# Optimization experiments

Measured on AMD Instinct MI355X. Metric: run time of the kernel, lower is better.

## Reference

```python
import jax, jax.numpy as jnp
import numpy as np

HEADS = 16

def setup_inputs() -> dict:
    key = jax.random.key(0)
    k1, k2, k3, k4 = jax.random.split(key, 4)
    B, S, D = 4, 2048, 1024
    x = jax.random.normal(k1, (B, S, D), dtype=jnp.float32)
    # original inits weights to constant 0.02; use small random init scaled similarly
    # to keep softmax non-degenerate while matching the module's math exactly.
    wq = jax.random.normal(k2, (D, D), dtype=jnp.float32) * 0.02
    wk = jax.random.normal(k3, (D, D), dtype=jnp.float32) * 0.02
    wv = jax.random.normal(k4, (D, D), dtype=jnp.float32) * 0.02
    return {"x": x, "wq": wq, "wk": wk, "wv": wv}

def reference(x, wq, wk, wv):
    B, S, D = x.shape
    H = HEADS
    hd = D // H
    # project and split heads: [B, S, D] -> [B, H, S, hd]
    q = (x @ wq).reshape(B, S, H, hd).transpose(0, 2, 1, 3)
    k = (x @ wk).reshape(B, S, H, hd).transpose(0, 2, 1, 3)
    v = (x @ wv).reshape(B, S, H, hd).transpose(0, 2, 1, 3)
    scores = jnp.einsum('bhid,bhjd->bhij', q, k) / jnp.sqrt(jnp.float32(hd))
    attn = jax.nn.softmax(scores, axis=-1)
    out = jnp.einsum('bhij,bhjd->bhid', attn, v)
    return out.transpose(0, 2, 1, 3).reshape(B, S, D)
```

## Files before the change

### kernel.cpp

```cpp
#include <hip/hip_runtime.h>
#include <hip/hip_bf16.h>
#include <stdint.h>


typedef __hip_bfloat16 bf16;
typedef __attribute__((ext_vector_type(8))) short short8;
typedef __attribute__((ext_vector_type(4))) float f32x4;
typedef __attribute__((ext_vector_type(4))) unsigned int u32x4;
typedef __attribute__((ext_vector_type(8))) unsigned short ushort8;

#define MFMA_16x16x32(a, b, c) __builtin_amdgcn_mfma_f32_16x16x32_bf16((a), (b), (c), 0, 0, 0)

__device__ __forceinline__ void gload_lds16(const void* g, void* l) {
  __builtin_amdgcn_global_load_lds((const __attribute__((address_space(1))) unsigned int*)g,
                                   (__attribute__((address_space(3))) unsigned int*)l,
                                   16, 0, 0);
}

__device__ __forceinline__ unsigned short bfu(float f) {
  return __bfloat16_as_ushort(__float2bfloat16(f));
}
__device__ __forceinline__ unsigned int pack2(float lo, float hi) {
  unsigned int r;
  asm("v_cvt_pk_bf16_f32 %0, %1, %2" : "=v"(r) : "v"(lo), "v"(hi));
  return r;
}
__device__ __forceinline__ float exp2_fast(float x) {
  float r;
  asm("v_exp_f32 %0, %1" : "=v"(r) : "v"(x));
  return r;
}

__global__ __launch_bounds__(256) void cvt_all_kernel(const float* __restrict__ x,
                                                      const float* __restrict__ w0,
                                                      const float* __restrict__ w1,
                                                      const float* __restrict__ w2,
                                                      bf16* __restrict__ xbf,
                                                      bf16* __restrict__ wT) {
  __shared__ float tile[64][65];
  const int t = threadIdx.x;
  const int bid = blockIdx.x;
  if (bid < 4096) {
    int i = bid * 256 + t;
    const float4* xv = (const float4*)x;
    float4 a = xv[i * 2];
    float4 b = xv[i * 2 + 1];
    ushort8 o;
    o[0] = bfu(a.x); o[1] = bfu(a.y); o[2] = bfu(a.z); o[3] = bfu(a.w);
    o[4] = bfu(b.x); o[5] = bfu(b.y); o[6] = bfu(b.z); o[7] = bfu(b.w);
    ((ushort8*)xbf)[i] = o;
    return;
  }
  const int wb = bid - 4096;
  const int mat = wb >> 8;
  const int rem = wb & 255;
  const int k0 = (rem >> 4) * 64;
  const int n0 = (rem & 15) * 64;
  const float* w = (mat == 0) ? w0 : ((mat == 1) ? w1 : w2);
#pragma unroll
  for (int it = 0; it < 4; ++it) {
    int lin = it * 1024 + t * 4;
    int row = lin >> 6, col = lin & 63;
    float4 v = *(const float4*)&w[(size_t)(k0 + row) * 1024 + n0 + col];
    tile[row][col] = v.x; tile[row][col + 1] = v.y;
    tile[row][col + 2] = v.z; tile[row][col + 3] = v.w;
  }
  __syncthreads();
#pragma unroll
  for (int it = 0; it < 2; ++it) {
    int chunk = it * 256 + t;
    int nrow = chunk >> 3, kc = chunk & 7;
    ushort8 o;
#pragma unroll
    for (int j = 0; j < 8; ++j) o[j] = bfu(tile[kc * 8 + j][nrow]);
    *(ushort8*)&wT[((size_t)mat * 1024 + n0 + nrow) * 1024 + k0 + kc * 8] = o;
  }
}

__global__ __launch_bounds__(256) void qkv_gemm_kernel(const bf16* __restrict__ A,
                                                       const bf16* __restrict__ Wt,
                                                       bf16* __restrict__ qb,
                                                       bf16* __restrict__ kb,
                                                       bf16* __restrict__ vtb) {
  __shared__ bf16 As[128 * 32];
  __shared__ bf16 Bs[128 * 32];
  const int t = threadIdx.x;
  const int w = t >> 6;
  const int lane = t & 63;
  const int G = lane >> 4, lq = lane & 15;
  const int m0 = blockIdx.y * 128;
  const int n0 = blockIdx.x * 128;
  const int wr = w >> 1, wc = w & 1;

  const f32x4 fzero = {0.f, 0.f, 0.f, 0.f};
  f32x4 acc[4][4];
#pragma unroll
  for (int i = 0; i < 4; ++i)
#pragma unroll
    for (int j = 0; j < 4; ++j) acc[i][j] = fzero;

  const int crow = t >> 2;
  const int ckc = t & 3;

  for (int k0 = 0; k0 < 1024; k0 += 32) {
#pragma unroll
    for (int rep = 0; rep < 2; ++rep) {
      int row = rep * 64 + crow;
      gload_lds16(&A[(size_t)(m0 + row) * 1024 + k0 + ckc * 8],
                  &As[(size_t)(rep * 256 + w * 64) * 8]);
      gload_lds16(&Wt[(size_t)(n0 + row) * 1024 + k0 + ckc * 8],
                  &Bs[(size_t)(rep * 256 + w * 64) * 8]);
    }
    __syncthreads();
    short8 af[4], bfr[4];
#pragma unroll
    for (int i = 0; i < 4; ++i)
      af[i] = *(const short8*)&As[(wr * 64 + i * 16 + lq) * 32 + G * 8];
#pragma unroll
    for (int j = 0; j < 4; ++j)
      bfr[j] = *(const short8*)&Bs[(wc * 64 + j * 16 + lq) * 32 + G * 8];
#pragma unroll
    for (int i = 0; i < 4; ++i)
#pragma unroll
      for (int j = 0; j < 4; ++j)
        acc[i][j] = MFMA_16x16x32(af[i], bfr[j], acc[i][j]);
    __syncthreads();
  }

  const int matid = n0 >> 10;
  const int nb = n0 & 1023;
#pragma unroll
  for (int i = 0; i < 4; ++i) {
#pragma unroll
    for (int r = 0; r < 4; ++r) {
      int mm = m0 + wr * 64 + i * 16 + G * 4 + r;
      int b = mm >> 11, s = mm & 2047;
#pragma unroll
      for (int j = 0; j < 4; ++j) {
        int nn = nb + wc * 64 + j * 16 + lq;
        int h = nn >> 6, d = nn & 63;
        float c = acc[i][j][r];
        size_t pb = (size_t)(b * 16 + h);
        if (matid == 0)
          qb[(pb * 2048 + s) * 64 + d] = __float2bfloat16(c * 0.18033688011112f);
        else if (matid == 1)
          kb[(pb * 2048 + s) * 64 + d] = __float2bfloat16(c);
        else
          vtb[(pb * 64 + d) * 2048 + s] = __float2bfloat16(c);
      }
    }
  }
}

__global__ __launch_bounds__(256) void attn_kernel(const bf16* __restrict__ Q,
                                                   const bf16* __restrict__ K,
                                                   const bf16* __restrict__ VT,
                                                   float* __restrict__ O) {
  __shared__ bf16 Kb[2][4096];
  __shared__ bf16 Vb[2][4096];
  const int t = threadIdx.x;
  const int w = t >> 6, lane = t & 63;
  const int G = lane >> 4, lq = lane & 15;
  const int sw = lq & 7;
  const int bid = blockIdx.x;
  const int pair = (((bid >> 7) & 7) << 3) | (bid & 7);
  const int chunk = (bid >> 3) & 15;
  const int b = pair >> 4, h = pair & 15;
  const size_t base = (size_t)pair * (2048 * 64);
  const int q0 = chunk * 128 + w * 32;

  const f32x4 fzero = {0.f, 0.f, 0.f, 0.f};
  short8 ones;
#pragma unroll
  for (int j = 0; j < 8; ++j) ones[j] = (short)0x3F80;

  const int srow = t >> 3, sbc = t & 7;
  const int ssc = (sbc ^ (srow & 7)) * 8;
  const int kprow = ((srow & 12) << 1) | ((srow & 16) >> 2) | (srow & 3);

#define STAGE_TILE(kvbase, bufi)                                                   \
  do {                                                                             \
    gload_lds16(&K[base + (size_t)((kvbase) + kprow) * 64 + ssc],                  \
                &Kb[bufi][(size_t)(w * 64) * 8]);                                  \
    gload_lds16(&K[base + (size_t)((kvbase) + 32 + kprow) * 64 + ssc],             \
                &Kb[bufi][(size_t)(256 + w * 64) * 8]);                            \
    gload_lds16(&VT[base + (size_t)srow * 2048 + (kvbase) + ssc],                  \
                &Vb[bufi][(size_t)(w * 64) * 8]);                                  \
    gload_lds16(&VT[base + (size_t)(32 + srow) * 2048 + (kvbase) + ssc],           \
                &Vb[bufi][(size_t)(256 + w * 64) * 8]);                            \
  } while (0)

#define TILE_COMPUTE(BUF)                                                          \
  _Pragma("unroll")                                                                \
  for (int h2 = 0; h2 < 2; ++h2) {                                                 \
    short8 kf0[2], kf1[2], vf[4];                                                  \
    _Pragma("unroll")                                                              \
    for (int hf = 0; hf < 2; ++hf) {                                               \
      kf0[hf] = *(const short8*)&Kb[BUF][((h2 * 2 + 0) * 16 + lq) * 64 + ((hf * 4 + G) ^ sw) * 8]; \
      kf1[hf] = *(const short8*)&Kb[BUF][((h2 * 2 + 1) * 16 + lq) * 64 + ((hf * 4 + G) ^ sw) * 8]; \
    }                                                                              \
    _Pragma("unroll")                                                              \
    for (int dt = 0; dt < 4; ++dt)                                                 \
      vf[dt] = *(const short8*)&Vb[BUF][(dt * 16 + lq) * 64 + ((h2 * 4 + G) ^ sw) * 8]; \
    _Pragma("unroll")                                                              \
    for (int qt = 0; qt < 2; ++qt) {                                               \
      f32x4 s0 = MFMA_16x16x32(kf0[0], qf[qt][0], fzero);                          \
      s0 = MFMA_16x16x32(kf0[1], qf[qt][1], s0);                                   \
      f32x4 s1 = MFMA_16x16x32(kf1[0], qf[qt][0], fzero);                          \
      s1 = MFMA_16x16x32(kf1[1], qf[qt][1], s1);                                   \
      u32x4 pw;                                                                    \
      pw[0] = pack2(exp2_fast(s0[0]), exp2_fast(s0[1]));                           \
      pw[1] = pack2(exp2_fast(s0[2]), exp2_fast(s0[3]));                           \
      pw[2] = pack2(exp2_fast(s1[0]), exp2_fast(s1[1]));                           \
      pw[3] = pack2(exp2_fast(s1[2]), exp2_fast(s1[3]));                           \
      short8 pf = __builtin_bit_cast(short8, pw);                                  \
      lacc[qt] = MFMA_16x16x32(ones, pf, lacc[qt]);                                \
      _Pragma("unroll")                                                            \
      for (int dt = 0; dt < 4; ++dt)                                               \
        acc[qt][dt] = MFMA_16x16x32(vf[dt], pf, acc[qt][dt]);                      \
    }                                                                              \
  }

  short8 qf[2][2];
#pragma unroll
  for (int qt = 0; qt < 2; ++qt)
#pragma unroll
    for (int hf = 0; hf < 2; ++hf)
      qf[qt][hf] = *(const short8*)&Q[base + (size_t)(q0 + qt * 16 + lq) * 64 + hf * 32 + G * 8];

  f32x4 acc[2][4];
#pragma unroll
  for (int qt = 0; qt < 2; ++qt)
#pragma unroll
    for (int dt = 0; dt < 4; ++dt) acc[qt][dt] = fzero;
  f32x4 lacc[2] = {fzero, fzero};

  STAGE_TILE(0, 0);
  __syncthreads();

  for (int it2 = 0; it2 < 16; ++it2) {
    const int kvc = it2 * 128;
    STAGE_TILE(kvc + 64, 1);
    TILE_COMPUTE(0)
    __syncthreads();
    if (it2 != 15) {
      STAGE_TILE(kvc + 128, 0);
    }
    TILE_COMPUTE(1)
    __syncthreads();
  }

#pragma unroll
  for (int qt = 0; qt < 2; ++qt) {
    float inv = 1.f / lacc[qt][0];
    size_t rowoff = ((size_t)b * 2048 + q0 + qt * 16 + lq) * 1024 + h * 64;
#pragma unroll
    for (int dt = 0; dt < 4; ++dt) {
      f32x4 o;
#pragma unroll
      for (int r = 0; r < 4; ++r) o[r] = acc[qt][dt][r] * inv;
      *(f32x4*)&O[rowoff + dt * 16 + G * 4] = o;
    }
  }
#undef STAGE_TILE
#undef TILE_COMPUTE
}

extern "C" void kernel_launch(void* const* d_in, const int* in_sizes, int n_in,
                              void* d_out, int out_size, void* d_ws, size_t ws_size,
                              hipStream_t stream) {
  const float* x = (const float*)d_in[0];
  const float* wq = (const float*)d_in[1];
  const float* wk = (const float*)d_in[2];
  const float* wv = (const float*)d_in[3];
  float* out = (float*)d_out;
  char* ws = (char*)d_ws;

  const size_t MB = 1024 * 1024;
  bf16* xbf = (bf16*)d_out;
  bf16* wT = (bf16*)(ws);
  bf16* qb = (bf16*)(ws + 6 * MB);
  bf16* kb = (bf16*)(ws + 22 * MB);
  bf16* vtb = (bf16*)(ws + 38 * MB);

  hipLaunchKernelGGL(cvt_all_kernel, dim3(4864), dim3(256), 0, stream,
                     x, wq, wk, wv, xbf, wT);
  hipLaunchKernelGGL(qkv_gemm_kernel, dim3(24, 64), dim3(256), 0, stream, xbf, wT, qb, kb, vtb);
  hipLaunchKernelGGL(attn_kernel, dim3(1024), dim3(256), 0, stream, qb, kb, vtb, out);
}
```

Baseline: 190.9 us.

## Swizzle QKV GEMM LDS layout, remap blocks per XCD, vectorize V-transpose stores

Three changes to the QKV projection GEMM. It XOR-swizzles the 16-byte chunk positions in the LDS tiles so the MFMA fragment reads avoid bank conflicts. It replaces the 2D grid with a 1D grid whose block index is mapped so each XCD works on a contiguous group of M tiles, which should improve L2 reuse of the A rows. It also writes the transposed V output as 4-element vectors instead of scalar stores, and it moves the Q/K/V branch out of the inner store loop.

```diff
diff --git a/kernel.cpp b/kernel.cpp
--- a/kernel.cpp
+++ b/kernel.cpp
@@ -8,6 +8,7 @@
 typedef __attribute__((ext_vector_type(4))) float f32x4;
 typedef __attribute__((ext_vector_type(4))) unsigned int u32x4;
 typedef __attribute__((ext_vector_type(8))) unsigned short ushort8;
+typedef __attribute__((ext_vector_type(4))) unsigned short ushort4v;
 
 #define MFMA_16x16x32(a, b, c) __builtin_amdgcn_mfma_f32_16x16x32_bf16((a), (b), (c), 0, 0, 0)
 
@@ -88,8 +89,10 @@
   const int w = t >> 6;
   const int lane = t & 63;
   const int G = lane >> 4, lq = lane & 15;
-  const int m0 = blockIdx.y * 128;
-  const int n0 = blockIdx.x * 128;
+  const int bid = blockIdx.x;
+  const int xcd = bid & 7, p = bid >> 3;
+  const int m0 = (xcd * 8 + (p & 7)) * 128;
+  const int n0 = (p >> 3) * 128;
   const int wr = w >> 1, wc = w & 1;
 
   const f32x4 fzero = {0.f, 0.f, 0.f, 0.f};
@@ -101,24 +104,26 @@
 
   const int crow = t >> 2;
   const int ckc = t & 3;
+  const int scs = (ckc ^ ((crow >> 1) & 3)) * 8;
+  const int fx = (lq >> 1) & 3;
 
   for (int k0 = 0; k0 < 1024; k0 += 32) {
 #pragma unroll
     for (int rep = 0; rep < 2; ++rep) {
       int row = rep * 64 + crow;
-      gload_lds16(&A[(size_t)(m0 + row) * 1024 + k0 + ckc * 8],
+      gload_lds16(&A[(size_t)(m0 + row) * 1024 + k0 + scs],
                   &As[(size_t)(rep * 256 + w * 64) * 8]);
-      gload_lds16(&Wt[(size_t)(n0 + row) * 1024 + k0 + ckc * 8],
+      gload_lds16(&Wt[(size_t)(n0 + row) * 1024 + k0 + scs],
                   &Bs[(size_t)(rep * 256 + w * 64) * 8]);
     }
     __syncthreads();
     short8 af[4], bfr[4];
 #pragma unroll
     for (int i = 0; i < 4; ++i)
-      af[i] = *(const short8*)&As[(wr * 64 + i * 16 + lq) * 32 + G * 8];
+      af[i] = *(const short8*)&As[(wr * 64 + i * 16 + lq) * 32 + (G ^ fx) * 8];
 #pragma unroll
     for (int j = 0; j < 4; ++j)
-      bfr[j] = *(const short8*)&Bs[(wc * 64 + j * 16 + lq) * 32 + G * 8];
+      bfr[j] = *(const short8*)&Bs[(wc * 64 + j * 16 + lq) * 32 + (G ^ fx) * 8];
 #pragma unroll
     for (int i = 0; i < 4; ++i)
 #pragma unroll
@@ -129,24 +134,37 @@
 
   const int matid = n0 >> 10;
   const int nb = n0 & 1023;
-#pragma unroll
-  for (int i = 0; i < 4; ++i) {
-#pragma unroll
-    for (int r = 0; r < 4; ++r) {
-      int mm = m0 + wr * 64 + i * 16 + G * 4 + r;
+  if (matid == 2) {
+#pragma unroll
+    for (int i = 0; i < 4; ++i) {
+      int mm = m0 + wr * 64 + i * 16 + G * 4;
       int b = mm >> 11, s = mm & 2047;
 #pragma unroll
       for (int j = 0; j < 4; ++j) {
         int nn = nb + wc * 64 + j * 16 + lq;
         int h = nn >> 6, d = nn & 63;
-        float c = acc[i][j][r];
-        size_t pb = (size_t)(b * 16 + h);
-        if (matid == 0)
-          qb[(pb * 2048 + s) * 64 + d] = __float2bfloat16(c * 0.18033688011112f);
-        else if (matid == 1)
-          kb[(pb * 2048 + s) * 64 + d] = __float2bfloat16(c);
-        else
-          vtb[(pb * 64 + d) * 2048 + s] = __float2bfloat16(c);
+        ushort4v o;
+#pragma unroll
+        for (int r = 0; r < 4; ++r) o[r] = bfu(acc[i][j][r]);
+        *(ushort4v*)&vtb[((size_t)(b * 16 + h) * 64 + d) * 2048 + s] = o;
+      }
+    }
+  } else {
+    const float scale = (matid == 0) ? 0.18033688011112f : 1.0f;
+    bf16* dst = (matid == 0) ? qb : kb;
+#pragma unroll
+    for (int i = 0; i < 4; ++i) {
+#pragma unroll
+      for (int r = 0; r < 4; ++r) {
+        int mm = m0 + wr * 64 + i * 16 + G * 4 + r;
+        int b = mm >> 11, s = mm & 2047;
+#pragma unroll
+        for (int j = 0; j < 4; ++j) {
+          int nn = nb + wc * 64 + j * 16 + lq;
+          int h = nn >> 6, d = nn & 63;
+          dst[((size_t)(b * 16 + h) * 2048 + s) * 64 + d] =
+              __float2bfloat16(acc[i][j][r] * scale);
+        }
       }
     }
   }
@@ -285,6 +303,6 @@
 
   hipLaunchKernelGGL(cvt_all_kernel, dim3(4864), dim3(256), 0, stream,
                      x, wq, wk, wv, xbf, wT);
-  hipLaunchKernelGGL(qkv_gemm_kernel, dim3(24, 64), dim3(256), 0, stream, xbf, wT, qb, kb, vtb);
+  hipLaunchKernelGGL(qkv_gemm_kernel, dim3(1536), dim3(256), 0, stream, xbf, wT, qb, kb, vtb);
   hipLaunchKernelGGL(attn_kernel, dim3(1024), dim3(256), 0, stream, qb, kb, vtb, out);
 }
```

Result: faster. 160.3 us (-16.0%).
